# Performance work log

Measured on AMD Instinct MI355X. Metric: run time of the kernel, lower is better.

The kernel has to match this reference:

```python
import jax, jax.numpy as jnp
import numpy as np

N_NODES = 100000
N_EDGES = 1000000
D = 64
N_GRAPHS = 512


def setup_inputs() -> dict:
    key = jax.random.key(0)
    k1, k2, k3, k4, k5 = jax.random.split(key, 5)
    x = jax.random.normal(k1, (N_NODES, D), dtype=jnp.float32)
    edge_index = jax.random.randint(k2, (2, N_EDGES), 0, N_NODES, dtype=jnp.int64)
    edge_attr = jax.random.uniform(k3, (N_EDGES,), dtype=jnp.float32)
    batch = jnp.sort(jax.random.randint(k4, (N_NODES,), 0, N_GRAPHS, dtype=jnp.int64))
    W = jax.random.normal(k5, (1, D), dtype=jnp.float32) / np.sqrt(D)
    b = jnp.zeros((1,), dtype=jnp.float32)
    return {"x": x, "edge_index": edge_index, "edge_attr": edge_attr, "batch": batch, "W": W, "b": b}


def reference(x, edge_index, edge_attr, batch, W, b):
    src, dst = edge_index[0], edge_index[1]
    # SimpleConv (aggr='sum'): out[v] = sum_{(u,v) in E} edge_attr_e * x[u]
    msgs = x[src] * edge_attr[:, None]                      # [E, D]
    agg = jax.ops.segment_sum(msgs, dst, num_segments=N_NODES)  # [N, D]
    # global_mean_pool over batch ids
    sums = jax.ops.segment_sum(agg, batch, num_segments=N_GRAPHS)  # [G, D]
    counts = jax.ops.segment_sum(jnp.ones((N_NODES,), dtype=x.dtype), batch, num_segments=N_GRAPHS)
    pooled = sums / jnp.maximum(counts, 1.0)[:, None]       # [G, D]
    # Linear(hidden_channels, 1)
    return pooled @ W.T + b                                 # [G, 1]
```

## Files before the change

### kernel.cpp

```cpp
#include <hip/hip_runtime.h>

#define N_NODES 100000
#define N_EDGES 1000000
#define D 64
#define N_GRAPHS 512

__global__ __launch_bounds__(256) void dot_kernel(const float* __restrict__ x,
                                                  const float* __restrict__ W,
                                                  float* __restrict__ y) {
    int t = blockIdx.x * blockDim.x + threadIdx.x;
    int v = t >> 4;
    int sub = t & 15;
    if (v >= N_NODES) return;
    const float4 xv = *reinterpret_cast<const float4*>(x + (size_t)v * D + sub * 4);
    const float4 wv = *reinterpret_cast<const float4*>(W + sub * 4);
    float p = xv.x * wv.x + xv.y * wv.y + xv.z * wv.z + xv.w * wv.w;
    p += __shfl_xor(p, 1, 64);
    p += __shfl_xor(p, 2, 64);
    p += __shfl_xor(p, 4, 64);
    p += __shfl_xor(p, 8, 64);
    if (sub == 0) y[v] = p;
}

__global__ __launch_bounds__(256) void edge_kernel(const int* __restrict__ ei,
                                                   const float* __restrict__ ea,
                                                   const int* __restrict__ batch,
                                                   const float* __restrict__ y,
                                                   float* __restrict__ acc) {
    __shared__ float sacc[N_GRAPHS];
    for (int i = threadIdx.x; i < N_GRAPHS; i += blockDim.x) sacc[i] = 0.0f;
    __syncthreads();
    const int* __restrict__ srcp = ei;
    const int* __restrict__ dstp = ei + N_EDGES;
    const int stride = gridDim.x * blockDim.x;
    for (int e = blockIdx.x * blockDim.x + threadIdx.x; e < N_EDGES; e += stride) {
        int s = srcp[e];
        int d = dstp[e];
        int g = batch[d];
        atomicAdd(&sacc[g], ea[e] * y[s]);
    }
    __syncthreads();
    for (int i = threadIdx.x; i < N_GRAPHS; i += blockDim.x) {
        float v = sacc[i];
        if (v != 0.0f) atomicAdd(&acc[i], v);
    }
}

__global__ __launch_bounds__(512) void final_kernel(const int* __restrict__ batch,
                                                    const float* __restrict__ acc,
                                                    const float* __restrict__ bptr,
                                                    float* __restrict__ out) {
    int g = threadIdx.x;
    int lo0 = 0, hi0 = N_NODES;
    while (lo0 < hi0) { int mid = (lo0 + hi0) >> 1; if (batch[mid] < g) lo0 = mid + 1; else hi0 = mid; }
    int lo1 = 0, hi1 = N_NODES;
    while (lo1 < hi1) { int mid = (lo1 + hi1) >> 1; if (batch[mid] < g + 1) lo1 = mid + 1; else hi1 = mid; }
    float cnt = (float)(hi1 - lo0);
    out[g] = acc[g] / fmaxf(cnt, 1.0f) + bptr[0];
}

extern "C" void kernel_launch(void* const* d_in, const int* in_sizes, int n_in,
                              void* d_out, int out_size, void* d_ws, size_t ws_size,
                              hipStream_t stream) {
    const float* x     = (const float*)d_in[0];
    const int*   ei    = (const int*)  d_in[1];
    const float* ea    = (const float*)d_in[2];
    const int*   batch = (const int*)  d_in[3];
    const float* W     = (const float*)d_in[4];
    const float* b     = (const float*)d_in[5];
    float* out = (float*)d_out;

    float* y   = (float*)d_ws;
    float* acc = y + N_NODES;

    hipMemsetAsync(acc, 0, N_GRAPHS * sizeof(float), stream);

    dot_kernel<<<(N_NODES * 16 + 255) / 256, 256, 0, stream>>>(x, W, y);
    edge_kernel<<<256, 256, 0, stream>>>(ei, ea, batch, y, acc);
    final_kernel<<<1, 512, 0, stream>>>(batch, acc, b, out);
}
```

Before: 109.6 us.

## Fuse memset and final kernel into dot and edge kernels with last-block finalize

Removes the memset and the single-block final kernel. Zeroing of acc and the per-graph count binary searches move into extra threads of the dot kernel. The edge kernel now uses 1024-thread blocks that each handle four edges through vectorized int4/float4 loads, and a last-block-done counter finalizes the output. This cuts launch overhead and serial tail work, at the cost of an atomic counter and thread fences.

Measured after the change: 170.5 us. 1.55x slower.

```diff
diff --git a/kernel.cpp b/kernel.cpp
--- a/kernel.cpp
+++ b/kernel.cpp
@@ -4,59 +4,93 @@
 #define N_EDGES 1000000
 #define D 64
 #define N_GRAPHS 512
+#define DOT_THREADS (N_NODES * 16)
+#define K2_BLOCKS 256
+#define K2_THREADS 1024
 
 __global__ __launch_bounds__(256) void dot_kernel(const float* __restrict__ x,
                                                   const float* __restrict__ W,
-                                                  float* __restrict__ y) {
+                                                  const int* __restrict__ batch,
+                                                  float* __restrict__ y,
+                                                  float* __restrict__ acc,
+                                                  float* __restrict__ inv_cnt,
+                                                  unsigned int* __restrict__ counter) {
     int t = blockIdx.x * blockDim.x + threadIdx.x;
-    int v = t >> 4;
-    int sub = t & 15;
-    if (v >= N_NODES) return;
-    const float4 xv = *reinterpret_cast<const float4*>(x + (size_t)v * D + sub * 4);
-    const float4 wv = *reinterpret_cast<const float4*>(W + sub * 4);
-    float p = xv.x * wv.x + xv.y * wv.y + xv.z * wv.z + xv.w * wv.w;
-    p += __shfl_xor(p, 1, 64);
-    p += __shfl_xor(p, 2, 64);
-    p += __shfl_xor(p, 4, 64);
-    p += __shfl_xor(p, 8, 64);
-    if (sub == 0) y[v] = p;
-}
-
-__global__ __launch_bounds__(256) void edge_kernel(const int* __restrict__ ei,
-                                                   const float* __restrict__ ea,
-                                                   const int* __restrict__ batch,
-                                                   const float* __restrict__ y,
-                                                   float* __restrict__ acc) {
-    __shared__ float sacc[N_GRAPHS];
-    for (int i = threadIdx.x; i < N_GRAPHS; i += blockDim.x) sacc[i] = 0.0f;
-    __syncthreads();
-    const int* __restrict__ srcp = ei;
-    const int* __restrict__ dstp = ei + N_EDGES;
-    const int stride = gridDim.x * blockDim.x;
-    for (int e = blockIdx.x * blockDim.x + threadIdx.x; e < N_EDGES; e += stride) {
-        int s = srcp[e];
-        int d = dstp[e];
-        int g = batch[d];
-        atomicAdd(&sacc[g], ea[e] * y[s]);
+    if (t < DOT_THREADS) {
+        int v = t >> 4;
+        int sub = t & 15;
+        const float4 xv = *reinterpret_cast<const float4*>(x + (size_t)v * D + sub * 4);
+        const float4 wv = *reinterpret_cast<const float4*>(W + sub * 4);
+        float p = xv.x * wv.x + xv.y * wv.y + xv.z * wv.z + xv.w * wv.w;
+        p += __shfl_xor(p, 1, 64);
+        p += __shfl_xor(p, 2, 64);
+        p += __shfl_xor(p, 4, 64);
+        p += __shfl_xor(p, 8, 64);
+        if (sub == 0) y[v] = p;
+        return;
     }
-    __syncthreads();
-    for (int i = threadIdx.x; i < N_GRAPHS; i += blockDim.x) {
-        float v = sacc[i];
-        if (v != 0.0f) atomicAdd(&acc[i], v);
-    }
-}
-
-__global__ __launch_bounds__(512) void final_kernel(const int* __restrict__ batch,
-                                                    const float* __restrict__ acc,
-                                                    const float* __restrict__ bptr,
-                                                    float* __restrict__ out) {
-    int g = threadIdx.x;
+    int g = t - DOT_THREADS;
+    if (g >= N_GRAPHS) return;
+    if (g == 0) *counter = 0u;
+    acc[g] = 0.0f;
     int lo0 = 0, hi0 = N_NODES;
     while (lo0 < hi0) { int mid = (lo0 + hi0) >> 1; if (batch[mid] < g) lo0 = mid + 1; else hi0 = mid; }
     int lo1 = 0, hi1 = N_NODES;
     while (lo1 < hi1) { int mid = (lo1 + hi1) >> 1; if (batch[mid] < g + 1) lo1 = mid + 1; else hi1 = mid; }
     float cnt = (float)(hi1 - lo0);
-    out[g] = acc[g] / fmaxf(cnt, 1.0f) + bptr[0];
+    inv_cnt[g] = 1.0f / fmaxf(cnt, 1.0f);
+}
+
+__global__ __launch_bounds__(K2_THREADS) void edge_kernel(const int* __restrict__ ei,
+                                                          const float* __restrict__ ea,
+                                                          const int* __restrict__ batch,
+                                                          const float* __restrict__ y,
+                                                          const float* __restrict__ inv_cnt,
+                                                          const float* __restrict__ bptr,
+                                                          float* __restrict__ acc,
+                                                          unsigned int* __restrict__ counter,
+                                                          float* __restrict__ out) {
+    __shared__ float sacc[N_GRAPHS];
+    __shared__ int is_last;
+    const int tid = threadIdx.x;
+    if (tid < N_GRAPHS) sacc[tid] = 0.0f;
+    __syncthreads();
+
+    int idx = blockIdx.x * K2_THREADS + tid;
+    if (idx < N_EDGES / 4) {
+        const int4   s4 = reinterpret_cast<const int4*>(ei)[idx];
+        const int4   d4 = reinterpret_cast<const int4*>(ei + N_EDGES)[idx];
+        const float4 a4 = reinterpret_cast<const float4*>(ea)[idx];
+        float m0 = a4.x * y[s4.x];  int g0 = batch[d4.x];
+        float m1 = a4.y * y[s4.y];  int g1 = batch[d4.y];
+        float m2 = a4.z * y[s4.z];  int g2 = batch[d4.z];
+        float m3 = a4.w * y[s4.w];  int g3 = batch[d4.w];
+        atomicAdd(&sacc[g0], m0);
+        atomicAdd(&sacc[g1], m1);
+        atomicAdd(&sacc[g2], m2);
+        atomicAdd(&sacc[g3], m3);
+    }
+    __syncthreads();
+    if (tid < N_GRAPHS) {
+        float v = sacc[tid];
+        if (v != 0.0f) atomicAdd(&acc[tid], v);
+    }
+    __threadfence();
+    __syncthreads();
+    if (tid == 0) {
+        unsigned int old = __hip_atomic_fetch_add(counter, 1u, __ATOMIC_ACQ_REL,
+                                                  __HIP_MEMORY_SCOPE_AGENT);
+        is_last = (old == (unsigned int)(gridDim.x - 1));
+    }
+    __syncthreads();
+    if (is_last) {
+        __threadfence();
+        if (tid < N_GRAPHS) {
+            float v = __hip_atomic_load(&acc[tid], __ATOMIC_RELAXED,
+                                        __HIP_MEMORY_SCOPE_AGENT);
+            out[tid] = v * inv_cnt[tid] + bptr[0];
+        }
+    }
 }
 
 extern "C" void kernel_launch(void* const* d_in, const int* in_sizes, int n_in,
@@ -70,12 +104,13 @@
     const float* b     = (const float*)d_in[5];
     float* out = (float*)d_out;
 
-    float* y   = (float*)d_ws;
-    float* acc = y + N_NODES;
+    float* y        = (float*)d_ws;
+    float* acc      = y + N_NODES;
+    float* inv_cnt  = acc + N_GRAPHS;
+    unsigned int* counter = (unsigned int*)(inv_cnt + N_GRAPHS);
 
-    hipMemsetAsync(acc, 0, N_GRAPHS * sizeof(float), stream);
-
-    dot_kernel<<<(N_NODES * 16 + 255) / 256, 256, 0, stream>>>(x, W, y);
-    edge_kernel<<<256, 256, 0, stream>>>(ei, ea, batch, y, acc);
-    final_kernel<<<1, 512, 0, stream>>>(batch, acc, b, out);
+    dot_kernel<<<(DOT_THREADS + N_GRAPHS + 255) / 256, 256, 0, stream>>>(
+        x, W, batch, y, acc, inv_cnt, counter);
+    edge_kernel<<<K2_BLOCKS, K2_THREADS, 0, stream>>>(
+        ei, ea, batch, y, inv_cnt, b, acc, counter, out);
 }
```
